# Kernel tuning notes

Measured on AMD Instinct MI355X. Metric: run time of the kernel, lower is better.

The kernel has to match this reference:

```python
import jax, jax.numpy as jnp
import numpy as np

BS, N, C = 16, 4096, 32
HID, OUT = 16, 1
N_ORBS = 64


def _linear_init(key, fan_in, fan_out):
    # torch nn.Linear default: U(-1/sqrt(fan_in), 1/sqrt(fan_in)) for W and b
    kw, kb = jax.random.split(key)
    bound = 1.0 / np.sqrt(fan_in)
    W = jax.random.uniform(kw, (fan_in, fan_out), minval=-bound, maxval=bound, dtype=jnp.float32)
    b = jax.random.uniform(kb, (fan_out,), minval=-bound, maxval=bound, dtype=jnp.float32)
    return W, b


def setup_inputs() -> dict:
    key = jax.random.key(0)
    ks = jax.random.split(key, 8)
    coords = jax.random.normal(ks[0], (BS, N, 2, 2), dtype=jnp.float32)
    # orbit identifiers live at coords[:, :, 1, 1]; draw from a fixed discrete set
    orb_ids = jax.random.randint(ks[1], (BS, N), 0, N_ORBS).astype(jnp.float32)
    # guarantee all N_ORBS values appear so unique() has exactly N_ORBS entries
    orb_ids = orb_ids.at[0, :N_ORBS].set(jnp.arange(N_ORBS, dtype=jnp.float32))
    coords = coords.at[:, :, 1, 1].set(orb_ids)
    vals = jax.random.normal(ks[2], (BS, N, C), dtype=jnp.float32)
    mask = jax.random.bernoulli(ks[3], 0.9, (BS, N))
    W1, b1 = _linear_init(ks[4], C, HID)
    W2, b2 = _linear_init(ks[5], HID, HID)
    W3, b3 = _linear_init(ks[6], HID, OUT)
    return {"coords": coords, "vals": vals, "mask": mask,
            "W1": W1, "b1": b1, "W2": W2, "b2": b2, "W3": W3, "b3": b3,
            "n_orbs": N_ORBS}


def reference(coords, vals, mask, W1, b1, W2, b2, W3, b3, n_orbs):
    orb = coords[:, :, 1, 1]                              # (bs, n)
    # torch.unique over the whole tensor -> sorted global unique orbit values
    uniq = jnp.unique(orb, size=n_orbs)                   # (n_orbs,)
    # orbit-membership mask; einsum contraction over n == masked broadcast + sum(dim=1)
    orbs_mask = (orb[:, :, None] == uniq[None, None, :]).astype(vals.dtype)  # (bs, n, n_orbs)
    masked_vals = jnp.where(mask[..., None], vals, jnp.zeros((), vals.dtype))  # (bs, n, c)
    agg_orbs = jnp.einsum('bnk,bnc->bkc', orbs_mask, masked_vals)              # (bs, n_orbs, c)
    empty_orbs = agg_orbs.sum(axis=-1) == 0               # (bs, n_orbs)
    h = jax.nn.relu(agg_orbs @ W1 + b1)
    h = jax.nn.relu(h @ W2 + b2)
    transf = h @ W3 + b3                                  # (bs, n_orbs, out_dim)
    transf = jnp.where(empty_orbs[..., None], jnp.zeros((), transf.dtype), transf)
    return transf.sum(axis=1)                             # (bs, out_dim)
```

## Files before the change

kernel.cpp:

```cpp
#include <hip/hip_runtime.h>

#define BS     16
#define NPTS   4096
#define CH     32
#define HID    16
#define NORB   64
#define SLICES 32
#define PPB    (NPTS / SLICES)
#define ITERS  (PPB / 32)

__global__ __launch_bounds__(256) void gigp_agg(
    const float* __restrict__ coords,
    const float* __restrict__ vals,
    const int*   __restrict__ mask,
    float*       __restrict__ part)
{
    __shared__ float agg[NORB][CH + 1];

    const int tid   = threadIdx.x;
    const int b     = blockIdx.x >> 5;
    const int slice = blockIdx.x & (SLICES - 1);

    for (int i = tid; i < NORB * (CH + 1); i += 256)
        (&agg[0][0])[i] = 0.0f;

    const int c4 = tid & 7;
    const int pl = tid >> 3;
    const float4* vals4 = (const float4*)vals;

    int    kk[ITERS];
    int    mm[ITERS];
    float4 vv[ITERS];
    #pragma unroll
    for (int it = 0; it < ITERS; ++it) {
        const int n  = slice * PPB + it * 32 + pl;
        const int gi = b * NPTS + n;
        kk[it] = (int)coords[(size_t)gi * 4 + 3];
        mm[it] = mask[gi];
        vv[it] = vals4[(size_t)gi * 8 + c4];
    }
    __syncthreads();

    #pragma unroll
    for (int it = 0; it < ITERS; ++it) {
        if (mm[it]) {
            const int k = kk[it];
            atomicAdd(&agg[k][c4 * 4 + 0], vv[it].x);
            atomicAdd(&agg[k][c4 * 4 + 1], vv[it].y);
            atomicAdd(&agg[k][c4 * 4 + 2], vv[it].z);
            atomicAdd(&agg[k][c4 * 4 + 3], vv[it].w);
        }
    }
    __syncthreads();

    float4* dst = (float4*)(part + ((size_t)b * SLICES + slice) * NORB * CH);
    #pragma unroll
    for (int j = 0; j < 2; ++j) {
        const int e  = tid + j * 256;
        const int k  = e >> 3;
        const int c4v = e & 7;
        float4 t;
        t.x = agg[k][c4v * 4 + 0];
        t.y = agg[k][c4v * 4 + 1];
        t.z = agg[k][c4v * 4 + 2];
        t.w = agg[k][c4v * 4 + 3];
        dst[e] = t;
    }
}

__global__ __launch_bounds__(256) void gigp_mlp(
    const float* __restrict__ part,
    const float* __restrict__ W1, const float* __restrict__ b1,
    const float* __restrict__ W2, const float* __restrict__ b2,
    const float* __restrict__ W3, const float* __restrict__ b3,
    float*       __restrict__ out)
{
    __shared__ float agg[NORB][CH + 1];

    const int b   = blockIdx.x;
    const int tid = threadIdx.x;

    const float4* src = (const float4*)(part + (size_t)b * SLICES * NORB * CH);

    float4 a0 = make_float4(0.f, 0.f, 0.f, 0.f);
    float4 a1 = make_float4(0.f, 0.f, 0.f, 0.f);
    #pragma unroll
    for (int s = 0; s < SLICES; ++s) {
        const float4 t0 = src[(size_t)s * (NORB * CH / 4) + tid];
        const float4 t1 = src[(size_t)s * (NORB * CH / 4) + tid + 256];
        a0.x += t0.x; a0.y += t0.y; a0.z += t0.z; a0.w += t0.w;
        a1.x += t1.x; a1.y += t1.y; a1.z += t1.z; a1.w += t1.w;
    }
    {
        const int e0 = tid, e1 = tid + 256;
        const int k0 = e0 >> 3, c0 = (e0 & 7) * 4;
        const int k1 = e1 >> 3, c1 = (e1 & 7) * 4;
        agg[k0][c0 + 0] = a0.x; agg[k0][c0 + 1] = a0.y;
        agg[k0][c0 + 2] = a0.z; agg[k0][c0 + 3] = a0.w;
        agg[k1][c1 + 0] = a1.x; agg[k1][c1 + 1] = a1.y;
        agg[k1][c1 + 2] = a1.z; agg[k1][c1 + 3] = a1.w;
    }
    __syncthreads();

    if (tid < NORB) {
        const int k = tid;

        float chsum = 0.0f;
        #pragma unroll
        for (int cc = 0; cc < CH; ++cc) chsum += agg[k][cc];

        float h1[HID];
        #pragma unroll
        for (int j = 0; j < HID; ++j) h1[j] = b1[j];
        #pragma unroll
        for (int cc = 0; cc < CH; ++cc) {
            const float x = agg[k][cc];
            #pragma unroll
            for (int j = 0; j < HID; ++j)
                h1[j] += x * W1[cc * HID + j];
        }
        #pragma unroll
        for (int j = 0; j < HID; ++j) h1[j] = h1[j] > 0.0f ? h1[j] : 0.0f;

        float h2[HID];
        #pragma unroll
        for (int j = 0; j < HID; ++j) h2[j] = b2[j];
        #pragma unroll
        for (int i = 0; i < HID; ++i) {
            const float x = h1[i];
            #pragma unroll
            for (int j = 0; j < HID; ++j)
                h2[j] += x * W2[i * HID + j];
        }
        float o = b3[0];
        #pragma unroll
        for (int i = 0; i < HID; ++i) {
            const float x = h2[i] > 0.0f ? h2[i] : 0.0f;
            o += x * W3[i];
        }
        o = (chsum == 0.0f) ? 0.0f : o;

        #pragma unroll
        for (int off = 32; off > 0; off >>= 1)
            o += __shfl_down(o, off);
        if (k == 0) out[b] = o;
    }
}

extern "C" void kernel_launch(void* const* d_in, const int* in_sizes, int n_in,
                              void* d_out, int out_size, void* d_ws, size_t ws_size,
                              hipStream_t stream) {
    const float* coords = (const float*)d_in[0];
    const float* vals   = (const float*)d_in[1];
    const int*   mask   = (const int*)d_in[2];
    const float* W1     = (const float*)d_in[3];
    const float* b1     = (const float*)d_in[4];
    const float* W2     = (const float*)d_in[5];
    const float* b2     = (const float*)d_in[6];
    const float* W3     = (const float*)d_in[7];
    const float* b3     = (const float*)d_in[8];
    float* out  = (float*)d_out;
    float* part = (float*)d_ws;

    gigp_agg<<<BS * SLICES, 256, 0, stream>>>(coords, vals, mask, part);
    gigp_mlp<<<BS, 256, 0, stream>>>(part, W1, b1, W2, b2, W3, b3, out);
}
```

Before: 96.72 us.

## Fuse aggregation and MLP into a single kernel with one block per batch

Replaces the two-kernel design (sliced partial aggregation into workspace, then a reduction+MLP kernel) with one fused kernel. Each of the 16 batches gets a single 1024-thread block that streams all 4096 points through shared-memory atomics, then runs the MLP with weights staged in LDS. This removes the workspace round trip and the second launch, but it uses only 16 workgroups on a GPU with many CUs, so parallelism and memory bandwidth use drop sharply.

```diff
diff --git a/kernel.cpp b/kernel.cpp
--- a/kernel.cpp
+++ b/kernel.cpp
@@ -1,109 +1,80 @@
 #include <hip/hip_runtime.h>
 
-#define BS     16
-#define NPTS   4096
-#define CH     32
-#define HID    16
-#define NORB   64
-#define SLICES 32
-#define PPB    (NPTS / SLICES)
-#define ITERS  (PPB / 32)
+#define BS    16
+#define NPTS  4096
+#define CH    32
+#define HID   16
+#define NORB  64
+#define NTHR  1024
+#define PTS_PER_PASS (NTHR / 8)
+#define NPASS (NPTS / PTS_PER_PASS)
+#define CHUNK 8
 
-__global__ __launch_bounds__(256) void gigp_agg(
+__global__ __launch_bounds__(NTHR) void gigp_fused(
     const float* __restrict__ coords,
     const float* __restrict__ vals,
     const int*   __restrict__ mask,
-    float*       __restrict__ part)
-{
-    __shared__ float agg[NORB][CH + 1];
-
-    const int tid   = threadIdx.x;
-    const int b     = blockIdx.x >> 5;
-    const int slice = blockIdx.x & (SLICES - 1);
-
-    for (int i = tid; i < NORB * (CH + 1); i += 256)
-        (&agg[0][0])[i] = 0.0f;
-
-    const int c4 = tid & 7;
-    const int pl = tid >> 3;
-    const float4* vals4 = (const float4*)vals;
-
-    int    kk[ITERS];
-    int    mm[ITERS];
-    float4 vv[ITERS];
-    #pragma unroll
-    for (int it = 0; it < ITERS; ++it) {
-        const int n  = slice * PPB + it * 32 + pl;
-        const int gi = b * NPTS + n;
-        kk[it] = (int)coords[(size_t)gi * 4 + 3];
-        mm[it] = mask[gi];
-        vv[it] = vals4[(size_t)gi * 8 + c4];
-    }
-    __syncthreads();
-
-    #pragma unroll
-    for (int it = 0; it < ITERS; ++it) {
-        if (mm[it]) {
-            const int k = kk[it];
-            atomicAdd(&agg[k][c4 * 4 + 0], vv[it].x);
-            atomicAdd(&agg[k][c4 * 4 + 1], vv[it].y);
-            atomicAdd(&agg[k][c4 * 4 + 2], vv[it].z);
-            atomicAdd(&agg[k][c4 * 4 + 3], vv[it].w);
-        }
-    }
-    __syncthreads();
-
-    float4* dst = (float4*)(part + ((size_t)b * SLICES + slice) * NORB * CH);
-    #pragma unroll
-    for (int j = 0; j < 2; ++j) {
-        const int e  = tid + j * 256;
-        const int k  = e >> 3;
-        const int c4v = e & 7;
-        float4 t;
-        t.x = agg[k][c4v * 4 + 0];
-        t.y = agg[k][c4v * 4 + 1];
-        t.z = agg[k][c4v * 4 + 2];
-        t.w = agg[k][c4v * 4 + 3];
-        dst[e] = t;
-    }
-}
-
-__global__ __launch_bounds__(256) void gigp_mlp(
-    const float* __restrict__ part,
     const float* __restrict__ W1, const float* __restrict__ b1,
     const float* __restrict__ W2, const float* __restrict__ b2,
     const float* __restrict__ W3, const float* __restrict__ b3,
     float*       __restrict__ out)
 {
     __shared__ float agg[NORB][CH + 1];
+    __shared__ float wbuf[832];
 
+    const int tid = threadIdx.x;
     const int b   = blockIdx.x;
-    const int tid = threadIdx.x;
 
-    const float4* src = (const float4*)(part + (size_t)b * SLICES * NORB * CH);
+    for (int i = tid; i < NORB * (CH + 1); i += NTHR)
+        (&agg[0][0])[i] = 0.0f;
 
-    float4 a0 = make_float4(0.f, 0.f, 0.f, 0.f);
-    float4 a1 = make_float4(0.f, 0.f, 0.f, 0.f);
-    #pragma unroll
-    for (int s = 0; s < SLICES; ++s) {
-        const float4 t0 = src[(size_t)s * (NORB * CH / 4) + tid];
-        const float4 t1 = src[(size_t)s * (NORB * CH / 4) + tid + 256];
-        a0.x += t0.x; a0.y += t0.y; a0.z += t0.z; a0.w += t0.w;
-        a1.x += t1.x; a1.y += t1.y; a1.z += t1.z; a1.w += t1.w;
-    }
-    {
-        const int e0 = tid, e1 = tid + 256;
-        const int k0 = e0 >> 3, c0 = (e0 & 7) * 4;
-        const int k1 = e1 >> 3, c1 = (e1 & 7) * 4;
-        agg[k0][c0 + 0] = a0.x; agg[k0][c0 + 1] = a0.y;
-        agg[k0][c0 + 2] = a0.z; agg[k0][c0 + 3] = a0.w;
-        agg[k1][c1 + 0] = a1.x; agg[k1][c1 + 1] = a1.y;
-        agg[k1][c1 + 2] = a1.z; agg[k1][c1 + 3] = a1.w;
+    if      (tid < 512) wbuf[tid] = W1[tid];
+    else if (tid < 528) wbuf[tid] = b1[tid - 512];
+    else if (tid < 784) wbuf[tid] = W2[tid - 528];
+    else if (tid < 800) wbuf[tid] = b2[tid - 784];
+    else if (tid < 816) wbuf[tid] = W3[tid - 800];
+    else if (tid == 816) wbuf[816] = b3[0];
+
+    const int c4 = tid & 7;
+    const int pl = tid >> 3;
+    const float4* vals4 = (const float4*)vals;
+
+    __syncthreads();
+
+    #pragma unroll 1
+    for (int pass0 = 0; pass0 < NPASS; pass0 += CHUNK) {
+        int    kk[CHUNK];
+        int    mm[CHUNK];
+        float4 vv[CHUNK];
+        #pragma unroll
+        for (int j = 0; j < CHUNK; ++j) {
+            const int n  = (pass0 + j) * PTS_PER_PASS + pl;
+            const int gi = b * NPTS + n;
+            kk[j] = (int)coords[(size_t)gi * 4 + 3];
+            mm[j] = mask[gi];
+            vv[j] = vals4[(size_t)gi * 8 + c4];
+        }
+        #pragma unroll
+        for (int j = 0; j < CHUNK; ++j) {
+            if (mm[j]) {
+                const int k = kk[j];
+                atomicAdd(&agg[k][c4 * 4 + 0], vv[j].x);
+                atomicAdd(&agg[k][c4 * 4 + 1], vv[j].y);
+                atomicAdd(&agg[k][c4 * 4 + 2], vv[j].z);
+                atomicAdd(&agg[k][c4 * 4 + 3], vv[j].w);
+            }
+        }
     }
     __syncthreads();
 
     if (tid < NORB) {
         const int k = tid;
+        const float* Wl1 = wbuf;
+        const float* bl1 = wbuf + 512;
+        const float* Wl2 = wbuf + 528;
+        const float* bl2 = wbuf + 784;
+        const float* Wl3 = wbuf + 800;
+        const float  bl3 = wbuf[816];
 
         float chsum = 0.0f;
         #pragma unroll
@@ -111,32 +82,32 @@
 
         float h1[HID];
         #pragma unroll
-        for (int j = 0; j < HID; ++j) h1[j] = b1[j];
+        for (int j = 0; j < HID; ++j) h1[j] = bl1[j];
         #pragma unroll
         for (int cc = 0; cc < CH; ++cc) {
             const float x = agg[k][cc];
             #pragma unroll
             for (int j = 0; j < HID; ++j)
-                h1[j] += x * W1[cc * HID + j];
+                h1[j] += x * Wl1[cc * HID + j];
         }
         #pragma unroll
         for (int j = 0; j < HID; ++j) h1[j] = h1[j] > 0.0f ? h1[j] : 0.0f;
 
         float h2[HID];
         #pragma unroll
-        for (int j = 0; j < HID; ++j) h2[j] = b2[j];
+        for (int j = 0; j < HID; ++j) h2[j] = bl2[j];
         #pragma unroll
         for (int i = 0; i < HID; ++i) {
             const float x = h1[i];
             #pragma unroll
             for (int j = 0; j < HID; ++j)
-                h2[j] += x * W2[i * HID + j];
+                h2[j] += x * Wl2[i * HID + j];
         }
-        float o = b3[0];
+        float o = bl3;
         #pragma unroll
         for (int i = 0; i < HID; ++i) {
             const float x = h2[i] > 0.0f ? h2[i] : 0.0f;
-            o += x * W3[i];
+            o += x * Wl3[i];
         }
         o = (chsum == 0.0f) ? 0.0f : o;
 
@@ -159,9 +130,8 @@
     const float* b2     = (const float*)d_in[6];
     const float* W3     = (const float*)d_in[7];
     const float* b3     = (const float*)d_in[8];
-    float* out  = (float*)d_out;
-    float* part = (float*)d_ws;
+    float* out = (float*)d_out;
 
-    gigp_agg<<<BS * SLICES, 256, 0, stream>>>(coords, vals, mask, part);
-    gigp_mlp<<<BS, 256, 0, stream>>>(part, W1, b1, W2, b2, W3, b3, out);
+    gigp_fused<<<BS, NTHR, 0, stream>>>(coords, vals, mask,
+                                        W1, b1, W2, b2, W3, b3, out);
 }
```

Result: slower. 232.0 us (+139.9%).

## Replace LDS atomics with owner-computes orbit aggregation and stage MLP weights in LDS

Applied to the files above, without the earlier changes.

The aggregation kernel now stages each slice's vals and orbit ids into LDS. Each thread owns one (orbit, 8-channel) pair and scans all points, accumulating in registers only when the broadcast orbit id matches, so shared-memory atomics are gone. Slices per batch drop from 32 to 16, which halves the partial-sum traffic read by the MLP kernel, and the MLP weights are preloaded into LDS. The cost is redundant scanning: every thread inspects every point, and there are fewer blocks.

```diff
diff --git a/kernel.cpp b/kernel.cpp
--- a/kernel.cpp
+++ b/kernel.cpp
@@ -5,9 +5,8 @@
 #define CH     32
 #define HID    16
 #define NORB   64
-#define SLICES 32
+#define SLICES 16
 #define PPB    (NPTS / SLICES)
-#define ITERS  (PPB / 32)
 
 __global__ __launch_bounds__(256) void gigp_agg(
     const float* __restrict__ coords,
@@ -15,57 +14,54 @@
     const int*   __restrict__ mask,
     float*       __restrict__ part)
 {
-    __shared__ float agg[NORB][CH + 1];
+    __shared__ float vlds[PPB][CH];
+    __shared__ int   klds[PPB];
 
     const int tid   = threadIdx.x;
-    const int b     = blockIdx.x >> 5;
+    const int b     = blockIdx.x >> 4;
     const int slice = blockIdx.x & (SLICES - 1);
+    const size_t gbase = (size_t)b * NPTS + slice * PPB;
 
-    for (int i = tid; i < NORB * (CH + 1); i += 256)
-        (&agg[0][0])[i] = 0.0f;
+    const float4* v4  = (const float4*)vals + gbase * (CH / 4);
+    float4*       vl4 = (float4*)&vlds[0][0];
+    #pragma unroll
+    for (int i = 0; i < PPB * CH / (4 * 256); ++i)
+        vl4[tid + i * 256] = v4[tid + i * 256];
 
-    const int c4 = tid & 7;
-    const int pl = tid >> 3;
-    const float4* vals4 = (const float4*)vals;
-
-    int    kk[ITERS];
-    int    mm[ITERS];
-    float4 vv[ITERS];
-    #pragma unroll
-    for (int it = 0; it < ITERS; ++it) {
-        const int n  = slice * PPB + it * 32 + pl;
-        const int gi = b * NPTS + n;
-        kk[it] = (int)coords[(size_t)gi * 4 + 3];
-        mm[it] = mask[gi];
-        vv[it] = vals4[(size_t)gi * 8 + c4];
+    {
+        const size_t gi = gbase + tid;
+        const int k = (int)coords[gi * 4 + 3];
+        klds[tid] = mask[gi] ? k : NORB;
     }
     __syncthreads();
 
-    #pragma unroll
-    for (int it = 0; it < ITERS; ++it) {
-        if (mm[it]) {
-            const int k = kk[it];
-            atomicAdd(&agg[k][c4 * 4 + 0], vv[it].x);
-            atomicAdd(&agg[k][c4 * 4 + 1], vv[it].y);
-            atomicAdd(&agg[k][c4 * 4 + 2], vv[it].z);
-            atomicAdd(&agg[k][c4 * 4 + 3], vv[it].w);
+    const int myk  = tid >> 2;
+    const int c0   = (tid & 3) * 8;
+    const int lane = tid & 63;
+    const int wo_s = __builtin_amdgcn_readfirstlane((tid >> 6) << 4);
+
+    float acc[8] = {0, 0, 0, 0, 0, 0, 0, 0};
+
+    for (int base = 0; base < PPB; base += 64) {
+        const int kreg = klds[base + lane];
+        #pragma unroll 8
+        for (int j = 0; j < 64; ++j) {
+            const int kn = __builtin_amdgcn_readlane(kreg, j);
+            if ((unsigned)(kn - wo_s) < 16u) {
+                if (kn == myk) {
+                    const float4 u0 = *(const float4*)&vlds[base + j][c0];
+                    const float4 u1 = *(const float4*)&vlds[base + j][c0 + 4];
+                    acc[0] += u0.x; acc[1] += u0.y; acc[2] += u0.z; acc[3] += u0.w;
+                    acc[4] += u1.x; acc[5] += u1.y; acc[6] += u1.z; acc[7] += u1.w;
+                }
+            }
         }
     }
-    __syncthreads();
 
     float4* dst = (float4*)(part + ((size_t)b * SLICES + slice) * NORB * CH);
-    #pragma unroll
-    for (int j = 0; j < 2; ++j) {
-        const int e  = tid + j * 256;
-        const int k  = e >> 3;
-        const int c4v = e & 7;
-        float4 t;
-        t.x = agg[k][c4v * 4 + 0];
-        t.y = agg[k][c4v * 4 + 1];
-        t.z = agg[k][c4v * 4 + 2];
-        t.w = agg[k][c4v * 4 + 3];
-        dst[e] = t;
-    }
+    const int fi = myk * 8 + (tid & 3) * 2;
+    dst[fi]     = make_float4(acc[0], acc[1], acc[2], acc[3]);
+    dst[fi + 1] = make_float4(acc[4], acc[5], acc[6], acc[7]);
 }
 
 __global__ __launch_bounds__(256) void gigp_mlp(
@@ -76,18 +72,28 @@
     float*       __restrict__ out)
 {
     __shared__ float agg[NORB][CH + 1];
-
+    __shared__ float wbuf[832];
     const int b   = blockIdx.x;
     const int tid = threadIdx.x;
 
+    for (int i = tid; i < 817; i += 256) {
+        float w;
+        if      (i < 512) w = W1[i];
+        else if (i < 528) w = b1[i - 512];
+        else if (i < 784) w = W2[i - 528];
+        else if (i < 800) w = b2[i - 784];
+        else if (i < 816) w = W3[i - 800];
+        else              w = b3[0];
+        wbuf[i] = w;
+    }
+
     const float4* src = (const float4*)(part + (size_t)b * SLICES * NORB * CH);
-
     float4 a0 = make_float4(0.f, 0.f, 0.f, 0.f);
     float4 a1 = make_float4(0.f, 0.f, 0.f, 0.f);
     #pragma unroll
     for (int s = 0; s < SLICES; ++s) {
-        const float4 t0 = src[(size_t)s * (NORB * CH / 4) + tid];
-        const float4 t1 = src[(size_t)s * (NORB * CH / 4) + tid + 256];
+        const float4 t0 = src[s * (NORB * CH / 4) + tid];
+        const float4 t1 = src[s * (NORB * CH / 4) + tid + 256];
         a0.x += t0.x; a0.y += t0.y; a0.z += t0.z; a0.w += t0.w;
         a1.x += t1.x; a1.y += t1.y; a1.z += t1.z; a1.w += t1.w;
     }
@@ -104,6 +110,12 @@
 
     if (tid < NORB) {
         const int k = tid;
+        const float* Wl1 = wbuf;
+        const float* bl1 = wbuf + 512;
+        const float* Wl2 = wbuf + 528;
+        const float* bl2 = wbuf + 784;
+        const float* Wl3 = wbuf + 800;
+        const float  bl3 = wbuf[816];
 
         float chsum = 0.0f;
         #pragma unroll
@@ -111,32 +123,32 @@
 
         float h1[HID];
         #pragma unroll
-        for (int j = 0; j < HID; ++j) h1[j] = b1[j];
+        for (int j = 0; j < HID; ++j) h1[j] = bl1[j];
         #pragma unroll
         for (int cc = 0; cc < CH; ++cc) {
             const float x = agg[k][cc];
             #pragma unroll
             for (int j = 0; j < HID; ++j)
-                h1[j] += x * W1[cc * HID + j];
+                h1[j] += x * Wl1[cc * HID + j];
         }
         #pragma unroll
         for (int j = 0; j < HID; ++j) h1[j] = h1[j] > 0.0f ? h1[j] : 0.0f;
 
         float h2[HID];
         #pragma unroll
-        for (int j = 0; j < HID; ++j) h2[j] = b2[j];
+        for (int j = 0; j < HID; ++j) h2[j] = bl2[j];
         #pragma unroll
         for (int i = 0; i < HID; ++i) {
             const float x = h1[i];
             #pragma unroll
             for (int j = 0; j < HID; ++j)
-                h2[j] += x * W2[i * HID + j];
+                h2[j] += x * Wl2[i * HID + j];
         }
-        float o = b3[0];
+        float o = bl3;
         #pragma unroll
         for (int i = 0; i < HID; ++i) {
             const float x = h2[i] > 0.0f ? h2[i] : 0.0f;
-            o += x * W3[i];
+            o += x * Wl3[i];
         }
         o = (chsum == 0.0f) ? 0.0f : o;
 
```

After: 98.05 us. Within noise of the previous version (+1.4%).
